# Performance work log

Measured on AMD Instinct MI355X. Metric: run time of the kernel, lower is better.

The kernel has to match this reference:

```python
import jax, jax.numpy as jnp
import numpy as np

N_NODES = 2048   # n_nodes; also ChebConv in/out channels (feature dim F == N)
C = 2            # n_data_per_node
K = 2            # cheby_kernel_size
E = 65536        # number of edges (avg degree 32)


def setup_inputs() -> dict:
    key = jax.random.key(0)
    k0, k1, k2, k3, k4 = jax.random.split(key, 5)
    x = jax.random.normal(k0, (N_NODES, C, N_NODES), dtype=jnp.float32)
    edge_index = jax.random.randint(k1, (2, E), 0, N_NODES)
    edge_weight = jax.random.uniform(k2, (E,), dtype=jnp.float32)
    # Stacked ChebConv params: one (K, F_in, F_out) Theta and (F_out,) bias per (i, j) pair.
    W = jax.random.normal(k3, (C, C, K, N_NODES, N_NODES), dtype=jnp.float32) * 0.02
    b = jax.random.normal(k4, (C, C, N_NODES), dtype=jnp.float32) * 0.02
    return {"x": x, "edge_index": edge_index, "edge_weight": edge_weight, "W": W, "b": b}


def _cheb_norm(edge_index, edge_weight, n):
    # PyG ChebConv normalization with normalization='sym', lambda_max=2.0:
    # L_hat = (2/lmax)*(I - D^-1/2 A D^-1/2) - I = -D^-1/2 A D^-1/2 (diagonal term is 0).
    row, col = edge_index[0], edge_index[1]
    deg = jnp.zeros((n,), edge_weight.dtype).at[row].add(edge_weight)
    safe = jnp.where(deg > 0, deg, 1.0)
    dis = jnp.where(deg > 0, jax.lax.rsqrt(safe), 0.0)
    return -dis[row] * edge_weight * dis[col]


def _propagate(x, row, col, w):
    # x: (B, N, C, F). Gather from source nodes (row), scatter-add into target nodes (col).
    msg = w[None, :, None, None] * x[:, row]          # (B, E, C, F)
    return jnp.zeros_like(x).at[:, col].add(msg)


def reference(x, edge_index, edge_weight, W, b):
    x_ = x[None]                                      # (1, N, C, F), F == N
    row, col = edge_index[0], edge_index[1]
    w = _cheb_norm(edge_index, edge_weight, x.shape[0])
    # Chebyshev recursion, shared across all input channels j simultaneously.
    Tx0 = x_
    Tx1 = _propagate(Tx0, row, col, w)
    Txs = [Tx0, Tx1]
    for _ in range(2, K):
        Txs.append(2.0 * _propagate(Txs[-1], row, col, w) - Txs[-2])
    Txs = jnp.stack(Txs)                              # (K, B, N, C, F)
    # y[:, :, i, :] = relu( sum_j ( sum_k Tx_k[..., j, :] @ W[i, j, k] + b[i, j] ) )
    y = jnp.einsum('kbnjf,ijkfg->bnig', Txs, W) + jnp.sum(b, axis=1)
    return jax.nn.relu(y)                             # (1, N, C, F)
```

## Files before the change

kernel.cpp:

```cpp
#include <hip/hip_runtime.h>

#define N_NODES 2048
#define EDGES   65536

typedef __bf16 bf16x8 __attribute__((ext_vector_type(8)));
typedef float  f32x4  __attribute__((ext_vector_type(4)));

typedef __attribute__((address_space(1))) const unsigned int gu32;
typedef __attribute__((address_space(3))) unsigned int lu32;

__device__ __forceinline__ void gll16(const void* g, void* l) {
  __builtin_amdgcn_global_load_lds((gu32*)g, (lu32*)l, 16, 0, 0);
}

__device__ __forceinline__ unsigned short f2bf(float f) {
  unsigned u = __builtin_bit_cast(unsigned, f);
  unsigned r = u + 0x7FFFu + ((u >> 16) & 1u);
  return (unsigned short)(r >> 16);
}
__device__ __forceinline__ float bf2f(unsigned short h) {
  return __builtin_bit_cast(float, (unsigned)h << 16);
}
__device__ __forceinline__ void split1(float f, unsigned short& hi, unsigned short& lo) {
  hi = f2bf(f);
  lo = f2bf(f - bf2f(hi));
}

__global__ void k_deg(const int* __restrict__ ei, const float* __restrict__ ew,
                      float* __restrict__ deg) {
  int e = blockIdx.x * 256 + threadIdx.x;
  atomicAdd(&deg[ei[e]], ew[e]);
}
__global__ void k_dis(const float* __restrict__ deg, float* __restrict__ dis) {
  int n = blockIdx.x * 256 + threadIdx.x;
  float d = deg[n];
  dis[n] = d > 0.f ? 1.f / sqrtf(d) : 0.f;
}
__global__ void k_scatterS(const int* __restrict__ ei, const float* __restrict__ ew,
                           const float* __restrict__ dis, float* __restrict__ S) {
  int e = blockIdx.x * 256 + threadIdx.x;
  int r = ei[e], c = ei[EDGES + e];
  float w = -dis[r] * ew[e] * dis[c];
  atomicAdd(&S[c * N_NODES + r], w);
}
__global__ void k_bsum(const float* __restrict__ b, float* __restrict__ bs) {
  int t = blockIdx.x * 256 + threadIdx.x;
  int i = t >> 11, g = t & 2047;
  bs[t] = b[(i * 2 + 0) * 2048 + g] + b[(i * 2 + 1) * 2048 + g];
}

__global__ void k_split(const float* __restrict__ in, unsigned short* __restrict__ hi,
                        unsigned short* __restrict__ lo) {
  int t = blockIdx.x * 256 + threadIdx.x;
  float4 v = ((const float4*)in)[t];
  ushort4 h, l;
  split1(v.x, h.x, l.x);
  split1(v.y, h.y, l.y);
  split1(v.z, h.z, l.z);
  split1(v.w, h.w, l.w);
  ((ushort4*)hi)[t] = h;
  ((ushort4*)lo)[t] = l;
}

template <int WMODE>
__global__ void k_tsplit(const float* __restrict__ in, unsigned short* __restrict__ oh,
                         unsigned short* __restrict__ ol) {
  __shared__ float tl[64][65];
  const int tid = threadIdx.x;
  int in_stride, out_stride;
  size_t in_base, out_base;
  if (WMODE == 0) {
    in_stride = 4096; out_stride = 2048; in_base = 0; out_base = 0;
  } else {
    in_stride = 2048; out_stride = 8192;
    int z = blockIdx.z;
    int i = z >> 2, j = (z >> 1) & 1, k = z & 1;
    in_base = (size_t)z << 22;
    out_base = (size_t)i * 2048 * 8192 + (size_t)(k * 2 + j) * 2048;
  }
  const int r0 = blockIdx.y * 64, c0 = blockIdx.x * 64;

#pragma unroll
  for (int q = 0; q < 4; ++q) {
    int s = q * 256 + tid;
    int row = s >> 4, c4 = (s & 15) * 4;
    float4 v = *(const float4*)(in + in_base + (size_t)(r0 + row) * in_stride + c0 + c4);
    tl[row][c4 + 0] = v.x; tl[row][c4 + 1] = v.y;
    tl[row][c4 + 2] = v.z; tl[row][c4 + 3] = v.w;
  }
  __syncthreads();
#pragma unroll
  for (int q = 0; q < 4; ++q) {
    int s = q * 256 + tid;
    int cc = s >> 4, rr = (s & 15) * 4;
    ushort4 h, l;
    split1(tl[rr + 0][cc], h.x, l.x);
    split1(tl[rr + 1][cc], h.y, l.y);
    split1(tl[rr + 2][cc], h.z, l.z);
    split1(tl[rr + 3][cc], h.w, l.w);
    size_t o = out_base + (size_t)(c0 + cc) * out_stride + r0 + rr;
    *(ushort4*)(oh + o) = h;
    *(ushort4*)(ol + o) = l;
  }
}

template <int MODE>
__global__ __launch_bounds__(256, 2)
void gemm_bf16(const unsigned short* __restrict__ Ah0, const unsigned short* __restrict__ Al0,
               const unsigned short* __restrict__ Ah1, const unsigned short* __restrict__ Al1,
               const unsigned short* __restrict__ Bh, const unsigned short* __restrict__ Bl,
               const float* __restrict__ bias,
               float* __restrict__ outF, unsigned short* __restrict__ outH,
               unsigned short* __restrict__ outL, int Kdim) {
  __shared__ unsigned short lds[4 * 4096];

  const int tid  = threadIdx.x;
  const int lane = tid & 63;
  const int wid  = tid >> 6;
  const int wr   = wid >> 1, wc = wid & 1;

  const int flat = blockIdx.y * 32 + blockIdx.x;
  const int swz  = (flat & 7) * 64 + (flat >> 3);
  const int n0   = (swz & 31) * 128;
  const int m0   = (swz >> 5) * 128;

  const int ldab = ((MODE == 0) ? 2048 : 4096) * 2;
  const int ldbb = ((MODE == 0) ? 2048 : 8192) * 2;

  const int srow = wid * 32 + (lane >> 2);
  const int kcl  = ((lane & 3) ^ ((lane >> 3) & 3)) * 16;
  const size_t rowA = (size_t)(m0 + srow) * ldab + kcl;
  const size_t rowB = (size_t)(n0 + srow) * ldbb + kcl;
  const int ldsc = wid * 2048;

  int arb[4], brb[4];
  const int physr = ((lane >> 4) ^ ((lane >> 1) & 3)) * 16;
#pragma unroll
  for (int mf = 0; mf < 4; ++mf)
    arb[mf] = (wr * 64 + mf * 16 + (lane & 15)) * 64 + physr;
#pragma unroll
  for (int nf = 0; nf < 4; ++nf)
    brb[nf] = (wc * 64 + nf * 16 + (lane & 15)) * 64 + physr;

  char* ldsb = (char*)lds;

  f32x4 acc[4][4] = {};

  for (int k0 = 0; k0 < Kdim; k0 += 32) {
    const char* bAh;
    const char* bAl;
    int kk = k0;
    if (MODE == 1 && k0 >= 4096) {
      bAh = (const char*)Ah1; bAl = (const char*)Al1; kk = k0 - 4096;
    } else {
      bAh = (const char*)Ah0; bAl = (const char*)Al0;
    }
    const size_t ka = rowA + (size_t)kk * 2;
    const size_t kb = rowB + (size_t)k0 * 2;
    const char* bBh = (const char*)Bh;
    const char* bBl = (const char*)Bl;

    __syncthreads();
#pragma unroll
    for (int q = 0; q < 2; ++q) {
      const size_t ra = ka + (size_t)q * 16 * ldab;
      const size_t rb = kb + (size_t)q * 16 * ldbb;
      const int dst = ldsc + q * 1024;
      gll16(bAh + ra, ldsb + 0 * 8192 + dst);
      gll16(bAl + ra, ldsb + 1 * 8192 + dst);
      gll16(bBh + rb, ldsb + 2 * 8192 + dst);
      gll16(bBl + rb, ldsb + 3 * 8192 + dst);
    }
    __syncthreads();

    bf16x8 ah[4], al[4], bh[4], bl[4];
#pragma unroll
    for (int mf = 0; mf < 4; ++mf) {
      ah[mf] = *(const bf16x8*)(ldsb + 0 * 8192 + arb[mf]);
      al[mf] = *(const bf16x8*)(ldsb + 1 * 8192 + arb[mf]);
    }
#pragma unroll
    for (int nf = 0; nf < 4; ++nf) {
      bh[nf] = *(const bf16x8*)(ldsb + 2 * 8192 + brb[nf]);
      bl[nf] = *(const bf16x8*)(ldsb + 3 * 8192 + brb[nf]);
    }
#pragma unroll
    for (int mf = 0; mf < 4; ++mf) {
#pragma unroll
      for (int nf = 0; nf < 4; ++nf) {
        acc[mf][nf] = __builtin_amdgcn_mfma_f32_16x16x32_bf16(ah[mf], bh[nf], acc[mf][nf], 0, 0, 0);
        acc[mf][nf] = __builtin_amdgcn_mfma_f32_16x16x32_bf16(ah[mf], bl[nf], acc[mf][nf], 0, 0, 0);
        acc[mf][nf] = __builtin_amdgcn_mfma_f32_16x16x32_bf16(al[mf], bh[nf], acc[mf][nf], 0, 0, 0);
      }
    }
  }

#pragma unroll
  for (int mf = 0; mf < 4; ++mf) {
#pragma unroll
    for (int nf = 0; nf < 4; ++nf) {
      int col = n0 + wc * 64 + nf * 16 + (lane & 15);
      float bv = (MODE == 1) ? bias[col] : 0.f;
#pragma unroll
      for (int r = 0; r < 4; ++r) {
        int row = m0 + wr * 64 + mf * 16 + ((lane >> 4) * 4) + r;
        size_t o = (size_t)row * 4096 + col;
        float v = acc[mf][nf][r];
        if (MODE == 1) {
          outF[o] = fmaxf(v + bv, 0.f);
        } else {
          unsigned short h, l;
          split1(v, h, l);
          outH[o] = h;
          outL[o] = l;
        }
      }
    }
  }
}

extern "C" void kernel_launch(void* const* d_in, const int* in_sizes, int n_in,
                              void* d_out, int out_size, void* d_ws, size_t ws_size,
                              hipStream_t stream) {
  const float* x  = (const float*)d_in[0];
  const int*   ei = (const int*)d_in[1];
  const float* ew = (const float*)d_in[2];
  const float* W  = (const float*)d_in[3];
  const float* b  = (const float*)d_in[4];
  float* out = (float*)d_out;

  char* ws = (char*)d_ws;
  float*          S     = (float*)(ws + 0);
  unsigned short* xT_hi = (unsigned short*)(ws + 16777216);
  unsigned short* xT_lo = (unsigned short*)(ws + 33554432);
  unsigned short* S_hi  = (unsigned short*)(ws + 50331648);
  unsigned short* S_lo  = (unsigned short*)(ws + 58720256);
  unsigned short* Wt_hi = (unsigned short*)(ws + 0);
  unsigned short* Wt_lo = (unsigned short*)(ws + 67108864);
  unsigned short* x_hi  = (unsigned short*)(ws + 134217728);
  unsigned short* x_lo  = (unsigned short*)(ws + 150994944);
  unsigned short* T_hi  = (unsigned short*)(ws + 167772160);
  unsigned short* T_lo  = (unsigned short*)(ws + 184549376);
  float*          deg   = (float*)(ws + 201326592);
  float*          dis   = (float*)(ws + 201334784);
  float*          bsum  = (float*)(ws + 201342976);

  hipMemsetAsync(S, 0, 16777216, stream);
  hipMemsetAsync(deg, 0, 8192, stream);

  k_deg<<<EDGES / 256, 256, 0, stream>>>(ei, ew, deg);
  k_dis<<<N_NODES / 256, 256, 0, stream>>>(deg, dis);
  k_scatterS<<<EDGES / 256, 256, 0, stream>>>(ei, ew, dis, S);
  k_bsum<<<4096 / 256, 256, 0, stream>>>(b, bsum);

  k_split<<<2097152 / 256, 256, 0, stream>>>(x, x_hi, x_lo);
  k_split<<<1048576 / 256, 256, 0, stream>>>(S, S_hi, S_lo);
  k_tsplit<0><<<dim3(64, 32, 1), 256, 0, stream>>>(x, xT_hi, xT_lo);

  dim3 grid(32, 16);
  gemm_bf16<0><<<grid, 256, 0, stream>>>(S_hi, S_lo, nullptr, nullptr,
                                         xT_hi, xT_lo, nullptr,
                                         nullptr, T_hi, T_lo, 2048);

  k_tsplit<1><<<dim3(32, 32, 8), 256, 0, stream>>>(W, Wt_hi, Wt_lo);

  gemm_bf16<1><<<grid, 256, 0, stream>>>(x_hi, x_lo, T_hi, T_lo,
                                         Wt_hi, Wt_lo, bsum,
                                         out, nullptr, nullptr, 8192);
}
```

Before: 908.8 us.

## Double-buffer LDS with prefetch and enlarge GEMM tile to 256x128 with 8 waves

The split-bf16 GEMM moves to 512-thread blocks, each computing a 256x128 output tile, so the grid halves and each CU runs one block. LDS is now double-buffered: the next K-slice is issued with global_load_lds while MFMAs run on the current slice, with explicit waitcnt, barriers and s_setprio around the MFMA block. The aim is to hide global-load latency, which the old single-buffer, two-barrier loop exposed, and to reuse the B tile across more rows. In exchange, occupancy drops to one block per CU and each block uses far more LDS.

```diff
diff --git a/kernel.cpp b/kernel.cpp
--- a/kernel.cpp
+++ b/kernel.cpp
@@ -105,33 +105,34 @@
 }
 
 template <int MODE>
-__global__ __launch_bounds__(256, 2)
+__global__ __launch_bounds__(512, 1)
 void gemm_bf16(const unsigned short* __restrict__ Ah0, const unsigned short* __restrict__ Al0,
                const unsigned short* __restrict__ Ah1, const unsigned short* __restrict__ Al1,
                const unsigned short* __restrict__ Bh, const unsigned short* __restrict__ Bl,
                const float* __restrict__ bias,
                float* __restrict__ outF, unsigned short* __restrict__ outH,
                unsigned short* __restrict__ outL, int Kdim) {
-  __shared__ unsigned short lds[4 * 4096];
+  __shared__ alignas(16) char lds[2 * 49152];
 
   const int tid  = threadIdx.x;
   const int lane = tid & 63;
   const int wid  = tid >> 6;
-  const int wr   = wid >> 1, wc = wid & 1;
+  const int wr   = wid >> 1;
+  const int wc   = wid & 1;
 
   const int flat = blockIdx.y * 32 + blockIdx.x;
-  const int swz  = (flat & 7) * 64 + (flat >> 3);
+  const int swz  = (flat & 7) * 32 + (flat >> 3);
   const int n0   = (swz & 31) * 128;
-  const int m0   = (swz >> 5) * 128;
+  const int m0   = (swz >> 5) * 256;
 
   const int ldab = ((MODE == 0) ? 2048 : 4096) * 2;
   const int ldbb = ((MODE == 0) ? 2048 : 8192) * 2;
 
-  const int srow = wid * 32 + (lane >> 2);
+  const int rsub = lane >> 2;
   const int kcl  = ((lane & 3) ^ ((lane >> 3) & 3)) * 16;
-  const size_t rowA = (size_t)(m0 + srow) * ldab + kcl;
-  const size_t rowB = (size_t)(n0 + srow) * ldbb + kcl;
-  const int ldsc = wid * 2048;
+  const size_t arow0 = (size_t)(m0 + wid * 32 + rsub) * ldab + kcl;
+  const size_t arow1 = (size_t)(m0 + wid * 32 + 16 + rsub) * ldab + kcl;
+  const size_t brow  = (size_t)(n0 + wid * 16 + rsub) * ldbb + kcl;
 
   int arb[4], brb[4];
   const int physr = ((lane >> 4) ^ ((lane >> 1) & 3)) * 16;
@@ -142,48 +143,52 @@
   for (int nf = 0; nf < 4; ++nf)
     brb[nf] = (wc * 64 + nf * 16 + (lane & 15)) * 64 + physr;
 
-  char* ldsb = (char*)lds;
+  auto STAGE = [&](int half, int k0) {
+    const char* pAh;
+    const char* pAl;
+    size_t ka;
+    if (MODE == 1 && k0 >= 4096) {
+      pAh = (const char*)Ah1; pAl = (const char*)Al1; ka = (size_t)(k0 - 4096) * 2;
+    } else {
+      pAh = (const char*)Ah0; pAl = (const char*)Al0; ka = (size_t)k0 * 2;
+    }
+    const size_t kb = (size_t)k0 * 2;
+    char* base = lds + half * 49152;
+    gll16(pAh + arow0 + ka, base + 0     + (2 * wid + 0) * 1024);
+    gll16(pAh + arow1 + ka, base + 0     + (2 * wid + 1) * 1024);
+    gll16(pAl + arow0 + ka, base + 16384 + (2 * wid + 0) * 1024);
+    gll16(pAl + arow1 + ka, base + 16384 + (2 * wid + 1) * 1024);
+    gll16((const char*)Bh + brow + kb, base + 32768 + wid * 1024);
+    gll16((const char*)Bl + brow + kb, base + 40960 + wid * 1024);
+  };
 
   f32x4 acc[4][4] = {};
-
-  for (int k0 = 0; k0 < Kdim; k0 += 32) {
-    const char* bAh;
-    const char* bAl;
-    int kk = k0;
-    if (MODE == 1 && k0 >= 4096) {
-      bAh = (const char*)Ah1; bAl = (const char*)Al1; kk = k0 - 4096;
-    } else {
-      bAh = (const char*)Ah0; bAl = (const char*)Al0;
-    }
-    const size_t ka = rowA + (size_t)kk * 2;
-    const size_t kb = rowB + (size_t)k0 * 2;
-    const char* bBh = (const char*)Bh;
-    const char* bBl = (const char*)Bl;
-
-    __syncthreads();
-#pragma unroll
-    for (int q = 0; q < 2; ++q) {
-      const size_t ra = ka + (size_t)q * 16 * ldab;
-      const size_t rb = kb + (size_t)q * 16 * ldbb;
-      const int dst = ldsc + q * 1024;
-      gll16(bAh + ra, ldsb + 0 * 8192 + dst);
-      gll16(bAl + ra, ldsb + 1 * 8192 + dst);
-      gll16(bBh + rb, ldsb + 2 * 8192 + dst);
-      gll16(bBl + rb, ldsb + 3 * 8192 + dst);
-    }
-    __syncthreads();
-
+  const int nt = Kdim / 32;
+
+  STAGE(0, 0);
+  asm volatile("s_waitcnt vmcnt(0)" ::: "memory");
+  __builtin_amdgcn_s_barrier();
+
+  int cur = 0;
+  for (int t = 0; t < nt; ++t) {
+    if (t + 1 < nt) STAGE(cur ^ 1, (t + 1) * 32);
+
+    const char* base = lds + cur * 49152;
     bf16x8 ah[4], al[4], bh[4], bl[4];
 #pragma unroll
     for (int mf = 0; mf < 4; ++mf) {
-      ah[mf] = *(const bf16x8*)(ldsb + 0 * 8192 + arb[mf]);
-      al[mf] = *(const bf16x8*)(ldsb + 1 * 8192 + arb[mf]);
+      ah[mf] = *(const bf16x8*)(base + arb[mf]);
+      al[mf] = *(const bf16x8*)(base + 16384 + arb[mf]);
     }
 #pragma unroll
     for (int nf = 0; nf < 4; ++nf) {
-      bh[nf] = *(const bf16x8*)(ldsb + 2 * 8192 + brb[nf]);
-      bl[nf] = *(const bf16x8*)(ldsb + 3 * 8192 + brb[nf]);
-    }
+      bh[nf] = *(const bf16x8*)(base + 32768 + brb[nf]);
+      bl[nf] = *(const bf16x8*)(base + 40960 + brb[nf]);
+    }
+    asm volatile("s_waitcnt lgkmcnt(0)" ::: "memory");
+    __builtin_amdgcn_sched_barrier(0);
+
+    __builtin_amdgcn_s_setprio(1);
 #pragma unroll
     for (int mf = 0; mf < 4; ++mf) {
 #pragma unroll
@@ -193,6 +198,11 @@
         acc[mf][nf] = __builtin_amdgcn_mfma_f32_16x16x32_bf16(al[mf], bh[nf], acc[mf][nf], 0, 0, 0);
       }
     }
+    __builtin_amdgcn_s_setprio(0);
+
+    asm volatile("s_waitcnt vmcnt(0)" ::: "memory");
+    __builtin_amdgcn_s_barrier();
+    cur ^= 1;
   }
 
 #pragma unroll
@@ -257,14 +267,14 @@
   k_split<<<1048576 / 256, 256, 0, stream>>>(S, S_hi, S_lo);
   k_tsplit<0><<<dim3(64, 32, 1), 256, 0, stream>>>(x, xT_hi, xT_lo);
 
-  dim3 grid(32, 16);
-  gemm_bf16<0><<<grid, 256, 0, stream>>>(S_hi, S_lo, nullptr, nullptr,
+  dim3 grid(32, 8);
+  gemm_bf16<0><<<grid, 512, 0, stream>>>(S_hi, S_lo, nullptr, nullptr,
                                          xT_hi, xT_lo, nullptr,
                                          nullptr, T_hi, T_lo, 2048);
 
   k_tsplit<1><<<dim3(32, 32, 8), 256, 0, stream>>>(W, Wt_hi, Wt_lo);
 
-  gemm_bf16<1><<<grid, 256, 0, stream>>>(x_hi, x_lo, T_hi, T_lo,
+  gemm_bf16<1><<<grid, 512, 0, stream>>>(x_hi, x_lo, T_hi, T_lo,
                                          Wt_hi, Wt_lo, bsum,
                                          out, nullptr, nullptr, 8192);
 }
```

Measured after the change: 821.8 us. -9.6%, faster.
